# Optimization experiments

Hardware: AMD Instinct MI355X
Metric: run time of the kernel (lower is better)

Reference implementation:

```python
import jax, jax.numpy as jnp
import numpy as np


def setup_inputs() -> dict:
    key = jax.random.key(0)
    k1, k2, k3, k4 = jax.random.split(key, 4)
    B, N, D, d_dir = 2, 512, 512, 64
    scale_in = 1.0 / np.sqrt(D)
    scale_dir = 1.0 / np.sqrt(d_dir)
    t = jax.random.normal(k1, (B, N, D), dtype=jnp.float32)
    Wq = jax.random.normal(k2, (d_dir, D), dtype=jnp.float32) * scale_in
    Wk = jax.random.normal(k3, (d_dir, D), dtype=jnp.float32) * scale_in
    Wv = jax.random.normal(k4, (D, d_dir), dtype=jnp.float32) * scale_dir
    return {"t": t, "Wq": Wq, "Wk": Wk, "Wv": Wv}


def reference(t, Wq, Wk, Wv):
    # t: (B, N, D); Wq, Wk: (d_dir, D); Wv: (D, d_dir)
    q = jnp.einsum('bnd,ed->bne', t, Wq)  # (B, N, d_dir)
    k = jnp.einsum('bnd,ed->bne', t, Wk)  # (B, N, d_dir)
    had = q[:, :, None, :] * k[:, None, :, :]  # (B, N, N, d_dir)
    kappa = jnp.einsum('bije,de->bijd', had, Wv)  # (B, N, N, D)
    return kappa
```

## Files before the change

### kernel.cpp

```cpp
#include <hip/hip_runtime.h>
#include <hip/hip_bf16.h>

#define NB   512
#define DB   512
#define EB   64
#define JT   16
#define TPB  16

typedef __bf16 bf16x8 __attribute__((ext_vector_type(8)));
typedef float  f32x4  __attribute__((ext_vector_type(4)));

__global__ __launch_bounds__(64) void qk_proj_bf16(
    const float* __restrict__ t,
    const float* __restrict__ Wq,
    const float* __restrict__ Wk,
    __bf16* __restrict__ qb,
    __bf16* __restrict__ kb)
{
    __shared__ float trow[DB];
    const int bn = blockIdx.x;
    const int e  = threadIdx.x;
    #pragma unroll
    for (int idx = 0; idx < DB / 64; ++idx)
        trow[idx * 64 + e] = t[(size_t)bn * DB + idx * 64 + e];
    __syncthreads();

    float aq = 0.f, ak = 0.f;
    const float* wqr = Wq + (size_t)e * DB;
    const float* wkr = Wk + (size_t)e * DB;
    #pragma unroll 8
    for (int d = 0; d < DB; ++d) {
        const float tv = trow[d];
        aq += tv * wqr[d];
        ak += tv * wkr[d];
    }
    qb[bn * EB + e] = (__bf16)aq;
    kb[bn * EB + e] = (__bf16)ak;
}

__global__ void wv_to_bf16(const float* __restrict__ Wv, __bf16* __restrict__ wvb, int n)
{
    int i = blockIdx.x * blockDim.x + threadIdx.x;
    if (i < n) wvb[i] = (__bf16)Wv[i];
}

__global__ __launch_bounds__(256) void kappa_mfma(
    const __bf16* __restrict__ qb,
    const __bf16* __restrict__ kb,
    const __bf16* __restrict__ wvb,
    float* __restrict__ out)
{
    const int blk = blockIdx.x;
    const int bi  = blk >> 1;
    const int b   = bi >> 9;
    const int jt0 = (blk & 1) * TPB;
    const int w    = threadIdx.x >> 6;
    const int l    = threadIdx.x & 63;
    const int lrow = l & 15;
    const int lgrp = l >> 4;
    const int dbase = w * 128;
    const int tid  = threadIdx.x;

    __shared__ float tile[JT * DB];

    bf16x8 bfrag[8][2];
    #pragma unroll
    for (int df = 0; df < 8; ++df) {
        const int d = dbase + df * 16 + lrow;
        #pragma unroll
        for (int ks = 0; ks < 2; ++ks)
            bfrag[df][ks] = *reinterpret_cast<const bf16x8*>(
                wvb + (size_t)d * EB + ks * 32 + lgrp * 8);
    }

    const bf16x8 qv0 = *reinterpret_cast<const bf16x8*>(qb + (size_t)bi * EB + lgrp * 8);
    const bf16x8 qv1 = *reinterpret_cast<const bf16x8*>(qb + (size_t)bi * EB + 32 + lgrp * 8);

    const __bf16* __restrict__ kbase = kb + (size_t)b * NB * EB;

    bf16x8 kv0 = *reinterpret_cast<const bf16x8*>(kbase + (size_t)(jt0 * JT + lrow) * EB + lgrp * 8);
    bf16x8 kv1 = *reinterpret_cast<const bf16x8*>(kbase + (size_t)(jt0 * JT + lrow) * EB + 32 + lgrp * 8);

    for (int t = 0; t < TPB; ++t) {
        bf16x8 a0, a1;
        #pragma unroll
        for (int x = 0; x < 8; ++x) {
            a0[x] = (__bf16)((float)kv0[x] * (float)qv0[x]);
            a1[x] = (__bf16)((float)kv1[x] * (float)qv1[x]);
        }

        f32x4 acc[8];
        #pragma unroll
        for (int df = 0; df < 8; ++df) {
            acc[df] = (f32x4){0.f, 0.f, 0.f, 0.f};
            acc[df] = __builtin_amdgcn_mfma_f32_16x16x32_bf16(bfrag[df][0], a0, acc[df], 0, 0, 0);
            acc[df] = __builtin_amdgcn_mfma_f32_16x16x32_bf16(bfrag[df][1], a1, acc[df], 0, 0, 0);
        }

        if (t + 1 < TPB) {
            const int jn = (jt0 + t + 1) * JT + lrow;
            kv0 = *reinterpret_cast<const bf16x8*>(kbase + (size_t)jn * EB + lgrp * 8);
            kv1 = *reinterpret_cast<const bf16x8*>(kbase + (size_t)jn * EB + 32 + lgrp * 8);
        }

        __syncthreads();

        #pragma unroll
        for (int df = 0; df < 8; ++df) {
            const int chunk = w * 32 + df * 4 + lgrp;
            const int swz   = chunk ^ (lrow & 7);
            *reinterpret_cast<f32x4*>(tile + lrow * DB + swz * 4) = acc[df];
        }

        __syncthreads();

        float* __restrict__ obase = out + ((size_t)bi * NB + (size_t)(jt0 + t) * JT) * DB;
        #pragma unroll
        for (int p = 0; p < 8; ++p) {
            const int f = p * 1024 + tid * 4;
            const int j = f >> 9;
            const int dchunk = (f >> 2) & 127;
            const int swz = dchunk ^ (j & 7);
            *reinterpret_cast<f32x4*>(obase + f) =
                *reinterpret_cast<const f32x4*>(tile + j * DB + swz * 4);
        }
    }
}

extern "C" void kernel_launch(void* const* d_in, const int* in_sizes, int n_in,
                              void* d_out, int out_size, void* d_ws, size_t ws_size,
                              hipStream_t stream) {
    const float* t  = (const float*)d_in[0];
    const float* Wq = (const float*)d_in[1];
    const float* Wk = (const float*)d_in[2];
    const float* Wv = (const float*)d_in[3];
    float* out = (float*)d_out;

    const int B = 2;

    __bf16* qb  = (__bf16*)d_ws;
    __bf16* kbf = qb + (size_t)B * NB * EB;
    __bf16* wvb = kbf + (size_t)B * NB * EB;

    qk_proj_bf16<<<dim3(B * NB), dim3(64), 0, stream>>>(t, Wq, Wk, qb, kbf);
    wv_to_bf16<<<dim3((DB * EB + 255) / 256), dim3(256), 0, stream>>>(Wv, wvb, DB * EB);

    kappa_mfma<<<dim3(2048), dim3(256), 0, stream>>>(qb, kbf, wvb, out);
}
```

Baseline: 238.5 us.

## Fold q into Wv fragments and use per-wave LDS tiles without block barriers

Premultiplies the Wv B-fragments by the per-row q vector once before the loop, so k fragments feed the MFMAs directly and the per-iteration elementwise multiply goes away. Splits the shared staging tile into one region per wavefront, with each wave storing only its own 128-column slice. This lets the two __syncthreads per iteration be replaced by compiler memory barriers. The cost is narrower per-wave output rows (512-byte row segments instead of full 2 KB rows), and the code relies on intra-wave LDS ordering without an explicit barrier. Rounding also changes slightly, since q*Wv is now rounded to bf16 instead of q*k.

```diff
diff --git a/kernel.cpp b/kernel.cpp
--- a/kernel.cpp
+++ b/kernel.cpp
@@ -59,42 +59,45 @@
     const int lrow = l & 15;
     const int lgrp = l >> 4;
     const int dbase = w * 128;
-    const int tid  = threadIdx.x;
 
-    __shared__ float tile[JT * DB];
+    __shared__ float lds[4 * JT * 128];
+    float* __restrict__ wtile = lds + w * (JT * 128);
+
+    const bf16x8 qv0 = *reinterpret_cast<const bf16x8*>(qb + (size_t)bi * EB + lgrp * 8);
+    const bf16x8 qv1 = *reinterpret_cast<const bf16x8*>(qb + (size_t)bi * EB + 32 + lgrp * 8);
 
     bf16x8 bfrag[8][2];
     #pragma unroll
     for (int df = 0; df < 8; ++df) {
         const int d = dbase + df * 16 + lrow;
         #pragma unroll
-        for (int ks = 0; ks < 2; ++ks)
-            bfrag[df][ks] = *reinterpret_cast<const bf16x8*>(
+        for (int ks = 0; ks < 2; ++ks) {
+            const bf16x8 wv = *reinterpret_cast<const bf16x8*>(
                 wvb + (size_t)d * EB + ks * 32 + lgrp * 8);
+            const bf16x8 qq = ks ? qv1 : qv0;
+            bf16x8 f;
+            #pragma unroll
+            for (int x = 0; x < 8; ++x)
+                f[x] = (__bf16)((float)wv[x] * (float)qq[x]);
+            bfrag[df][ks] = f;
+        }
     }
-
-    const bf16x8 qv0 = *reinterpret_cast<const bf16x8*>(qb + (size_t)bi * EB + lgrp * 8);
-    const bf16x8 qv1 = *reinterpret_cast<const bf16x8*>(qb + (size_t)bi * EB + 32 + lgrp * 8);
 
     const __bf16* __restrict__ kbase = kb + (size_t)b * NB * EB;
 
     bf16x8 kv0 = *reinterpret_cast<const bf16x8*>(kbase + (size_t)(jt0 * JT + lrow) * EB + lgrp * 8);
     bf16x8 kv1 = *reinterpret_cast<const bf16x8*>(kbase + (size_t)(jt0 * JT + lrow) * EB + 32 + lgrp * 8);
 
+    const int r_lo = l >> 5;
+    const int cc   = l & 31;
+
     for (int t = 0; t < TPB; ++t) {
-        bf16x8 a0, a1;
-        #pragma unroll
-        for (int x = 0; x < 8; ++x) {
-            a0[x] = (__bf16)((float)kv0[x] * (float)qv0[x]);
-            a1[x] = (__bf16)((float)kv1[x] * (float)qv1[x]);
-        }
-
         f32x4 acc[8];
         #pragma unroll
         for (int df = 0; df < 8; ++df) {
             acc[df] = (f32x4){0.f, 0.f, 0.f, 0.f};
-            acc[df] = __builtin_amdgcn_mfma_f32_16x16x32_bf16(bfrag[df][0], a0, acc[df], 0, 0, 0);
-            acc[df] = __builtin_amdgcn_mfma_f32_16x16x32_bf16(bfrag[df][1], a1, acc[df], 0, 0, 0);
+            acc[df] = __builtin_amdgcn_mfma_f32_16x16x32_bf16(bfrag[df][0], kv0, acc[df], 0, 0, 0);
+            acc[df] = __builtin_amdgcn_mfma_f32_16x16x32_bf16(bfrag[df][1], kv1, acc[df], 0, 0, 0);
         }
 
         if (t + 1 < TPB) {
@@ -103,26 +106,22 @@
             kv1 = *reinterpret_cast<const bf16x8*>(kbase + (size_t)jn * EB + 32 + lgrp * 8);
         }
 
-        __syncthreads();
-
+        asm volatile("" ::: "memory");
         #pragma unroll
         for (int df = 0; df < 8; ++df) {
-            const int chunk = w * 32 + df * 4 + lgrp;
-            const int swz   = chunk ^ (lrow & 7);
-            *reinterpret_cast<f32x4*>(tile + lrow * DB + swz * 4) = acc[df];
+            const int sc = (df * 4 + lgrp) ^ (lrow & 7);
+            *reinterpret_cast<f32x4*>(wtile + lrow * 128 + sc * 4) = acc[df];
         }
+        asm volatile("" ::: "memory");
 
-        __syncthreads();
-
-        float* __restrict__ obase = out + ((size_t)bi * NB + (size_t)(jt0 + t) * JT) * DB;
+        float* __restrict__ obase =
+            out + ((size_t)bi * NB + (size_t)(jt0 + t) * JT) * DB + dbase;
         #pragma unroll
         for (int p = 0; p < 8; ++p) {
-            const int f = p * 1024 + tid * 4;
-            const int j = f >> 9;
-            const int dchunk = (f >> 2) & 127;
-            const int swz = dchunk ^ (j & 7);
-            *reinterpret_cast<f32x4*>(obase + f) =
-                *reinterpret_cast<const f32x4*>(tile + j * DB + swz * 4);
+            const int r  = 2 * p + r_lo;
+            const int sc = cc ^ (r & 7);
+            const f32x4 v = *reinterpret_cast<const f32x4*>(wtile + r * 128 + sc * 4);
+            *reinterpret_cast<f32x4*>(obase + (size_t)r * DB + cc * 4) = v;
         }
     }
 }
```

Result: no change. 234.5 us (-1.7%).
